# Kernel optimization log

Measured on AMD Instinct MI355X. Metric: run time of the kernel, lower is better.

## Reference

```python
import jax, jax.numpy as jnp
import numpy as np

LN_EPS = 1e-5        # torch default LayerNorm eps
DEB_EPS = 1e-7       # deberta-v3 layer_norm_eps
ATT_SPAN = 256       # deberta-v3-base position_buckets -> pos_ebd_size
MAX_REL = 100        # config.max_relative_positions override


def _ln(x, g, b, eps):
    m = x.mean(-1, keepdims=True)
    v = jnp.var(x, axis=-1, keepdims=True)
    return (x - m) * jax.lax.rsqrt(v + eps) * g + b


def _lin(x, w, b):
    return x @ w.T + b


def _rel_buckets(L):
    # build_relative_position + make_log_bucket_position (bucket_size=256, max_position=100)
    rel = jnp.arange(L, dtype=jnp.int32)[:, None] - jnp.arange(L, dtype=jnp.int32)[None, :]
    mid = ATT_SPAN // 2
    sign = jnp.sign(rel)
    abs_pos = jnp.where((rel < mid) & (rel > -mid), mid - 1, jnp.abs(rel))
    log_pos = jnp.ceil(jnp.log(abs_pos.astype(jnp.float32) / mid)
                       / np.float32(np.log((MAX_REL - 1) / mid)) * (mid - 1)) + mid
    return jnp.where(abs_pos <= mid, rel, (log_pos * sign).astype(jnp.int32))


def _forward(ints, floats):
    type_ids, landmark_ids, mask = ints
    (xs, ys, zs, type_emb, landmark_emb, type_ln_g, type_ln_b, lm_ln_g, lm_ln_b,
     pos_w, pos_b, lt_in_w, lt_in_b, lt_out_w, lt_out_b, lt_ln1_g, lt_ln1_b,
     lt_ff1_w, lt_ff1_b, lt_ff2_w, lt_ff2_b, lt_ln2_g, lt_ln2_b,
     rel_emb, rel_ln_g, rel_ln_b, dq_w, dq_b, dk_w, dk_b, dv_w, dv_b,
     dao_w, dao_b, da_ln_g, da_ln_b, di_w, di_b, do_w, do_b, do_ln_g, do_ln_b,
     head_w, head_b) = floats

    # embeddings (padding_idx=0 -> zero row & zero grad) + layernorms + pos projection
    te = _ln(type_emb[type_ids] * (type_ids != 0)[..., None].astype(jnp.float32), type_ln_g, type_ln_b, LN_EPS)
    le = _ln(landmark_emb[landmark_ids] * (landmark_ids != 0)[..., None].astype(jnp.float32), lm_ln_g, lm_ln_b, LN_EPS)
    pe = _lin(jnp.stack([xs, ys, zs], -1), pos_w, pos_b)
    fts = jnp.concatenate([te, le, pe], -1)                  # [B,F,L,768]
    B, F, L, D = fts.shape
    h = fts.reshape(B * F, L, D)

    # --- nn.TransformerEncoderLayer over landmarks (post-norm, relu, nhead=1) ---
    q, k, v = jnp.split(_lin(h, lt_in_w, lt_in_b), 3, axis=-1)
    probs = jax.nn.softmax(jnp.einsum('bqd,bkd->bqk', q, k) / np.float32(np.sqrt(D)), axis=-1)
    attn = _lin(jnp.einsum('bqk,bkd->bqd', probs, v), lt_out_w, lt_out_b)
    h = _ln(h + attn, lt_ln1_g, lt_ln1_b, LN_EPS)
    ff = _lin(jax.nn.relu(_lin(h, lt_ff1_w, lt_ff1_b)), lt_ff2_w, lt_ff2_b)
    h = _ln(h + ff, lt_ln2_g, lt_ln2_b, LN_EPS)

    h = h.reshape(B, F, L, D).mean(2)                        # [B,F,768]

    # --- DebertaV2 layer over frames (disentangled attention, 1 head) ---
    m = mask[:, :, 0] > 0                                    # [B,F]
    q = _lin(h, dq_w, dq_b)
    k = _lin(h, dk_w, dk_b)
    v = _lin(h, dv_w, dv_b)
    scale = np.float32(np.sqrt(D * 3))                       # scale_factor = 1 + len({c2p,p2c})
    scores = jnp.einsum('bqd,bkd->bqk', q, k) / scale
    rel_ln = _ln(rel_emb, rel_ln_g, rel_ln_b, DEB_EPS)       # norm_rel_ebd='layer_norm'
    pos_q = _lin(rel_ln, dq_w, dq_b)                         # share_att_key=True
    pos_k = _lin(rel_ln, dk_w, dk_b)
    rel = _rel_buckets(F)                                    # [F,F]
    c2p_idx = jnp.clip(rel + ATT_SPAN, 0, 2 * ATT_SPAN - 1)
    c2p = jnp.einsum('bqd,rd->bqr', q, pos_k)                # [B,F,512]
    c2p = jnp.take_along_axis(c2p, jnp.broadcast_to(c2p_idx[None], (B, F, F)), axis=-1)
    p2c_idx = jnp.clip(-rel + ATT_SPAN, 0, 2 * ATT_SPAN - 1)
    p2c = jnp.einsum('bkd,rd->bkr', k, pos_q)                # [B,F,512]
    p2c = jnp.take_along_axis(p2c, jnp.broadcast_to(p2c_idx[None], (B, F, F)), axis=-1)
    scores = scores + (c2p + jnp.swapaxes(p2c, -1, -2)) / scale
    amask = m[:, :, None] & m[:, None, :]                    # XSoftmax mask
    probs = jax.nn.softmax(jnp.where(amask, scores, jnp.finfo(scores.dtype).min), axis=-1)
    probs = jnp.where(amask, probs, 0.0)
    ctx = jnp.einsum('bqk,bkd->bqd', probs, v)
    h = _ln(_lin(ctx, dao_w, dao_b) + h, da_ln_g, da_ln_b, DEB_EPS)
    inter = jax.nn.gelu(_lin(h, di_w, di_b), approximate=False)
    h = _ln(_lin(inter, do_w, do_b) + h, do_ln_g, do_ln_b, DEB_EPS)

    return _lin(h.mean(1), head_w, head_b)                   # [B,250]


def setup_inputs():
    ks = iter(jax.random.split(jax.random.key(0), 64))
    B, F, L, E, D, DF, NC = 8, 80, 100, 256, 768, 3072, 250
    def w(*shape):
        return jax.random.normal(next(ks), shape, dtype=jnp.float32) * 0.02
    z = lambda *s: jnp.zeros(s, jnp.float32)
    o = lambda *s: jnp.ones(s, jnp.float32)
    return {
        "type_ids": jax.random.randint(next(ks), (B, F, L), 0, 12, dtype=jnp.int32),
        "landmark_ids": jax.random.randint(next(ks), (B, F, L), 0, 127, dtype=jnp.int32),
        "xs": jax.random.normal(next(ks), (B, F, L), dtype=jnp.float32),
        "ys": jax.random.normal(next(ks), (B, F, L), dtype=jnp.float32),
        "zs": jax.random.normal(next(ks), (B, F, L), dtype=jnp.float32),
        "mask": jnp.ones((B, F, L), jnp.int32),
        "type_emb": w(12, E), "landmark_emb": w(127, E),
        "type_ln_g": o(E), "type_ln_b": z(E), "lm_ln_g": o(E), "lm_ln_b": z(E),
        "pos_w": w(E, 3), "pos_b": z(E),
        "lt_in_w": w(3 * D, D), "lt_in_b": z(3 * D), "lt_out_w": w(D, D), "lt_out_b": z(D),
        "lt_ln1_g": o(D), "lt_ln1_b": z(D),
        "lt_ff1_w": w(D, D), "lt_ff1_b": z(D), "lt_ff2_w": w(D, D), "lt_ff2_b": z(D),
        "lt_ln2_g": o(D), "lt_ln2_b": z(D),
        "rel_emb": w(2 * ATT_SPAN, D), "rel_ln_g": o(D), "rel_ln_b": z(D),
        "dq_w": w(D, D), "dq_b": z(D), "dk_w": w(D, D), "dk_b": z(D), "dv_w": w(D, D), "dv_b": z(D),
        "dao_w": w(D, D), "dao_b": z(D), "da_ln_g": o(D), "da_ln_b": z(D),
        "di_w": w(DF, D), "di_b": z(DF), "do_w": w(D, DF), "do_b": z(D),
        "do_ln_g": o(D), "do_ln_b": z(D),
        "head_w": w(NC, D), "head_b": z(NC),
    }


def reference(type_ids, landmark_ids, xs, ys, zs, mask, type_emb, landmark_emb,
              type_ln_g, type_ln_b, lm_ln_g, lm_ln_b, pos_w, pos_b,
              lt_in_w, lt_in_b, lt_out_w, lt_out_b, lt_ln1_g, lt_ln1_b,
              lt_ff1_w, lt_ff1_b, lt_ff2_w, lt_ff2_b, lt_ln2_g, lt_ln2_b,
              rel_emb, rel_ln_g, rel_ln_b, dq_w, dq_b, dk_w, dk_b, dv_w, dv_b,
              dao_w, dao_b, da_ln_g, da_ln_b, di_w, di_b, do_w, do_b,
              do_ln_g, do_ln_b, head_w, head_b):
    floats = (xs, ys, zs, type_emb, landmark_emb, type_ln_g, type_ln_b, lm_ln_g, lm_ln_b,
              pos_w, pos_b, lt_in_w, lt_in_b, lt_out_w, lt_out_b, lt_ln1_g, lt_ln1_b,
              lt_ff1_w, lt_ff1_b, lt_ff2_w, lt_ff2_b, lt_ln2_g, lt_ln2_b,
              rel_emb, rel_ln_g, rel_ln_b, dq_w, dq_b, dk_w, dk_b, dv_w, dv_b,
              dao_w, dao_b, da_ln_g, da_ln_b, di_w, di_b, do_w, do_b, do_ln_g, do_ln_b,
              head_w, head_b)
    return _forward((type_ids, landmark_ids, mask), floats)
```

## Files before the change

kernel.cpp:

```cpp
#include <hip/hip_runtime.h>

using short8v = __attribute__((ext_vector_type(8))) short;
using float4v = __attribute__((ext_vector_type(4))) float;

__device__ __forceinline__ unsigned short f2bf(float f) {
  unsigned int u = __float_as_uint(f);
  u += 0x7FFF + ((u >> 16) & 1);
  return (unsigned short)(u >> 16);
}
__device__ __forceinline__ float bf2f(unsigned short u) {
  return __uint_as_float((unsigned int)u << 16);
}

__device__ __forceinline__ int swz(int row, int c) {
  return row * 64 + (c ^ ((row & 7) << 3));
}

template<int BM, int ACT, bool OUTBF, int RES>
__global__ __launch_bounds__(256) void gemm_mfma(
    const unsigned short* __restrict__ A, const unsigned short* __restrict__ B,
    const float* __restrict__ bias, const void* __restrict__ resid, int ldr,
    void* __restrict__ Cv,
    int M, int N, int K, int lda, int ldb, int ldc,
    long long sA, long long sB, long long sC, long long sBias, float alpha)
{
  constexpr int NF = BM / 32;
  A += (long long)blockIdx.z * sA;
  B += (long long)blockIdx.z * sB;
  if (bias) bias += (long long)blockIdx.z * sBias;
  const int m0 = blockIdx.y * BM, n0 = blockIdx.x * BM;

  __shared__ __align__(16) unsigned short As[BM * 64];
  __shared__ __align__(16) unsigned short Bs[BM * 64];

  const int tid = threadIdx.x;
  const int w = tid >> 6, lane = tid & 63;
  const int wr = w >> 1, wc = w & 1;

  const int r0 = tid >> 3;
  const int c8 = (tid & 7) * 8;
  int ra[NF], rb[NF], soff[NF];
  #pragma unroll
  for (int i = 0; i < NF; ++i) {
    int r = m0 + r0 + i * 32; ra[i] = r < M - 1 ? r : M - 1;
    int q = n0 + r0 + i * 32; rb[i] = q < N - 1 ? q : N - 1;
    soff[i] = swz(r0 + i * 32, c8);
  }

  const int fr = lane & 15;
  const int fk = (lane >> 4) * 8;

  float4v acc[NF][NF] = {};

  short8v pa[NF], pb[NF];
  #pragma unroll
  for (int i = 0; i < NF; ++i) {
    pa[i] = *(const short8v*)(A + (long long)ra[i] * lda + c8);
    pb[i] = *(const short8v*)(B + (long long)rb[i] * ldb + c8);
  }

  for (int k0 = 0; k0 < K; k0 += 64) {
    __syncthreads();
    #pragma unroll
    for (int i = 0; i < NF; ++i) {
      *(short8v*)&As[soff[i]] = pa[i];
      *(short8v*)&Bs[soff[i]] = pb[i];
    }
    __syncthreads();
    if (k0 + 64 < K) {
      #pragma unroll
      for (int i = 0; i < NF; ++i) {
        pa[i] = *(const short8v*)(A + (long long)ra[i] * lda + k0 + 64 + c8);
        pb[i] = *(const short8v*)(B + (long long)rb[i] * ldb + k0 + 64 + c8);
      }
    }
    #pragma unroll
    for (int kk = 0; kk < 2; ++kk) {
      short8v a[NF], b[NF];
      #pragma unroll
      for (int i = 0; i < NF; ++i) {
        a[i] = *(const short8v*)&As[swz(wr * (NF * 16) + i * 16 + fr, kk * 32 + fk)];
        b[i] = *(const short8v*)&Bs[swz(wc * (NF * 16) + i * 16 + fr, kk * 32 + fk)];
      }
      #pragma unroll
      for (int mi = 0; mi < NF; ++mi)
        #pragma unroll
        for (int ni = 0; ni < NF; ++ni)
          acc[mi][ni] = __builtin_amdgcn_mfma_f32_16x16x32_bf16(a[mi], b[ni], acc[mi][ni], 0, 0, 0);
    }
  }

  const int ccol0 = n0 + wc * (NF * 16) + (lane & 15);
  const int crow0 = m0 + wr * (NF * 16) + (lane >> 4) * 4;
  float* Cf = (float*)Cv + (long long)blockIdx.z * sC;
  unsigned short* Cb = (unsigned short*)Cv + (long long)blockIdx.z * sC;
  #pragma unroll
  for (int ni = 0; ni < NF; ++ni) {
    const int col = ccol0 + ni * 16;
    if (col >= N) continue;
    const float bs = bias ? bias[col] : 0.f;
    #pragma unroll
    for (int mi = 0; mi < NF; ++mi) {
      #pragma unroll
      for (int r = 0; r < 4; ++r) {
        const int row = crow0 + mi * 16 + r;
        if (row >= M) continue;
        float v = acc[mi][ni][r] * alpha + bs;
        if (RES == 1) v += bf2f(((const unsigned short*)resid)[(long long)row * ldr + col]);
        if (RES == 2) v += ((const float*)resid)[(long long)row * ldr + col];
        if (ACT == 1) v = fmaxf(v, 0.f);
        if (ACT == 2) v = 0.5f * v * (1.f + erff(v * 0.70710678118654752f));
        if (OUTBF) Cb[(long long)row * ldc + col] = f2bf(v);
        else       Cf[(long long)row * ldc + col] = v;
      }
    }
  }
}

static void mg(hipStream_t st, int bm, int act, bool outbf, int res,
               const unsigned short* A, const unsigned short* B,
               const float* bias, const void* resid, int ldr, void* C,
               int M, int N, int K, int lda, int ldb, int ldc,
               long long sA, long long sB, long long sC, long long sBias,
               int bat, float alpha)
{
  dim3 grid((N + bm - 1) / bm, (M + bm - 1) / bm, bat);
  dim3 blk(256);
  #define GEMM_CALL(BM_, A_, O_, R_) \
    gemm_mfma<BM_, A_, O_, R_><<<grid, blk, 0, st>>>(A, B, bias, resid, ldr, C, \
        M, N, K, lda, ldb, ldc, sA, sB, sC, sBias, alpha)
  if (bm == 128) {
    if (outbf) {
      if (act == 1)       GEMM_CALL(128, 1, true, 0);
      else if (res == 1)  GEMM_CALL(128, 0, true, 1);
      else                GEMM_CALL(128, 0, true, 0);
    } else {
      GEMM_CALL(128, 0, false, 0);
    }
  } else {
    if (outbf) {
      if (act == 2)       GEMM_CALL(64, 2, true, 0);
      else                GEMM_CALL(64, 0, true, 0);
    } else {
      if (res == 2)       GEMM_CALL(64, 0, false, 2);
      else                GEMM_CALL(64, 0, false, 0);
    }
  }
  #undef GEMM_CALL
}

__global__ __launch_bounds__(256) void scoresm_kernel(
    const unsigned short* __restrict__ Q, const unsigned short* __restrict__ Kp,
    unsigned short* __restrict__ P,
    int Mv, int K, int lda, long long sQ, long long sP, float alpha)
{
  const int z = blockIdx.z;
  Q  += (long long)z * sQ;
  Kp += (long long)z * sQ;
  P  += (long long)z * sP;

  __shared__ __align__(16) unsigned short As[128 * 64];
  __shared__ __align__(16) unsigned short Bs[128 * 64];
  float* ovl = (float*)As;

  const int tid = threadIdx.x;
  const int w = tid >> 6, lane = tid & 63;
  const int wr = w >> 1, wc = w & 1;
  const int r0 = tid >> 3, c8 = (tid & 7) * 8;

  int ra[4], soff[4];
  #pragma unroll
  for (int i = 0; i < 4; ++i) {
    int r = r0 + i * 32;
    ra[i] = (r < Mv - 1 ? r : Mv - 1);
    soff[i] = swz(r, c8);
  }
  const int fr = lane & 15, fk = (lane >> 4) * 8;

  float4v acc[4][4] = {};
  short8v pa[4], pb[4];
  #pragma unroll
  for (int i = 0; i < 4; ++i) {
    pa[i] = *(const short8v*)(Q  + (long long)ra[i] * lda + c8);
    pb[i] = *(const short8v*)(Kp + (long long)ra[i] * lda + c8);
  }
  for (int k0 = 0; k0 < K; k0 += 64) {
    __syncthreads();
    #pragma unroll
    for (int i = 0; i < 4; ++i) {
      *(short8v*)&As[soff[i]] = pa[i];
      *(short8v*)&Bs[soff[i]] = pb[i];
    }
    __syncthreads();
    if (k0 + 64 < K) {
      #pragma unroll
      for (int i = 0; i < 4; ++i) {
        pa[i] = *(const short8v*)(Q  + (long long)ra[i] * lda + k0 + 64 + c8);
        pb[i] = *(const short8v*)(Kp + (long long)ra[i] * lda + k0 + 64 + c8);
      }
    }
    #pragma unroll
    for (int kk = 0; kk < 2; ++kk) {
      short8v a[4], b[4];
      #pragma unroll
      for (int i = 0; i < 4; ++i) {
        a[i] = *(const short8v*)&As[swz(wr * 64 + i * 16 + fr, kk * 32 + fk)];
        b[i] = *(const short8v*)&Bs[swz(wc * 64 + i * 16 + fr, kk * 32 + fk)];
      }
      #pragma unroll
      for (int mi = 0; mi < 4; ++mi)
        #pragma unroll
        for (int ni = 0; ni < 4; ++ni)
          acc[mi][ni] = __builtin_amdgcn_mfma_f32_16x16x32_bf16(a[mi], b[ni], acc[mi][ni], 0, 0, 0);
    }
  }
  __syncthreads();

  const int g = lane >> 4, f = lane & 15;
  const int colB = wc * 64 + f;
  const int rowB = wr * 64 + g * 4;

  bool cv[4];
  #pragma unroll
  for (int ni = 0; ni < 4; ++ni) cv[ni] = (colB + ni * 16) < Mv;

  float lm[4][4];
  #pragma unroll
  for (int mi = 0; mi < 4; ++mi) {
    #pragma unroll
    for (int r = 0; r < 4; ++r) {
      float mx = -3.4e38f;
      #pragma unroll
      for (int ni = 0; ni < 4; ++ni) {
        float v = cv[ni] ? acc[mi][ni][r] * alpha : -3.4e38f;
        acc[mi][ni][r] = v;
        mx = fmaxf(mx, v);
      }
      #pragma unroll
      for (int off = 1; off < 16; off <<= 1) mx = fmaxf(mx, __shfl_xor(mx, off, 64));
      lm[mi][r] = mx;
    }
  }
  if (f == 0) {
    #pragma unroll
    for (int mi = 0; mi < 4; ++mi)
      #pragma unroll
      for (int r = 0; r < 4; ++r)
        ovl[wc * 128 + rowB + mi * 16 + r] = lm[mi][r];
  }
  __syncthreads();
  float ls[4][4];
  #pragma unroll
  for (int mi = 0; mi < 4; ++mi) {
    #pragma unroll
    for (int r = 0; r < 4; ++r) {
      const int row = rowB + mi * 16 + r;
      const float m = fmaxf(lm[mi][r], ovl[(wc ^ 1) * 128 + row]);
      float s = 0.f;
      #pragma unroll
      for (int ni = 0; ni < 4; ++ni) {
        const float v = acc[mi][ni][r];
        const float e = (v > -1e37f) ? expf(v - m) : 0.f;
        acc[mi][ni][r] = e;
        s += e;
      }
      #pragma unroll
      for (int off = 1; off < 16; off <<= 1) s += __shfl_xor(s, off, 64);
      ls[mi][r] = s;
    }
  }
  if (f == 0) {
    #pragma unroll
    for (int mi = 0; mi < 4; ++mi)
      #pragma unroll
      for (int r = 0; r < 4; ++r)
        ovl[256 + wc * 128 + rowB + mi * 16 + r] = ls[mi][r];
  }
  __syncthreads();
  #pragma unroll
  for (int mi = 0; mi < 4; ++mi) {
    #pragma unroll
    for (int r = 0; r < 4; ++r) {
      const int row = rowB + mi * 16 + r;
      const float tot = ls[mi][r] + ovl[256 + (wc ^ 1) * 128 + row];
      const float inv = (tot > 0.f) ? 1.f / tot : 0.f;
      #pragma unroll
      for (int ni = 0; ni < 4; ++ni)
        P[(long long)row * 128 + colB + ni * 16] = f2bf(acc[mi][ni][r] * inv);
    }
  }
}

struct ConvArgs {
  const float* s[10];
  unsigned short* d[10];
  long long off[11];
};
__global__ __launch_bounds__(256) void convall_kernel(ConvArgs a, long long tot)
{
  const long long i = ((long long)blockIdx.x * 256 + threadIdx.x) * 4;
  if (i >= tot) return;
  int t = 0;
  while (i >= a.off[t + 1]) ++t;
  const long long j = i - a.off[t];
  const float4 v = *(const float4*)(a.s[t] + j);
  const unsigned int lo = (unsigned int)f2bf(v.x) | ((unsigned int)f2bf(v.y) << 16);
  const unsigned int hi = (unsigned int)f2bf(v.z) | ((unsigned int)f2bf(v.w) << 16);
  *(uint2*)(a.d[t] + j) = make_uint2(lo, hi);
}

__global__ __launch_bounds__(256) void embed_kernel(
    const int* __restrict__ tids, const int* __restrict__ lids,
    const float* __restrict__ xs, const float* __restrict__ ys, const float* __restrict__ zs,
    const float* __restrict__ temb, const float* __restrict__ lemb,
    const float* __restrict__ tg, const float* __restrict__ tb,
    const float* __restrict__ lg, const float* __restrict__ lb,
    const float* __restrict__ pw, const float* __restrict__ pb,
    unsigned short* __restrict__ hb)
{
  const int tok = blockIdx.x * 4 + (threadIdx.x >> 6);
  const int lane = threadIdx.x & 63;
  const int e0 = lane * 4;
  const int ti = tids[tok], li = lids[tok];
  float4 tv = make_float4(0.f, 0.f, 0.f, 0.f);
  float4 lv = make_float4(0.f, 0.f, 0.f, 0.f);
  if (ti != 0) tv = *(const float4*)(temb + ti * 256 + e0);
  if (li != 0) lv = *(const float4*)(lemb + li * 256 + e0);

  float s0 = tv.x + tv.y + tv.z + tv.w;
  float s1 = tv.x * tv.x + tv.y * tv.y + tv.z * tv.z + tv.w * tv.w;
  float s2 = lv.x + lv.y + lv.z + lv.w;
  float s3 = lv.x * lv.x + lv.y * lv.y + lv.z * lv.z + lv.w * lv.w;
  #pragma unroll
  for (int off = 32; off > 0; off >>= 1) {
    s0 += __shfl_xor(s0, off, 64);
    s1 += __shfl_xor(s1, off, 64);
    s2 += __shfl_xor(s2, off, 64);
    s3 += __shfl_xor(s3, off, 64);
  }
  const float mt = s0 * (1.f / 256.f), vt = s1 * (1.f / 256.f) - mt * mt;
  const float ml = s2 * (1.f / 256.f), vl = s3 * (1.f / 256.f) - ml * ml;
  const float rt = rsqrtf(vt + 1e-5f), rl = rsqrtf(vl + 1e-5f);

  const float4 tg4 = *(const float4*)(tg + e0), tb4 = *(const float4*)(tb + e0);
  const float4 lg4 = *(const float4*)(lg + e0), lb4 = *(const float4*)(lb + e0);
  const size_t base = (size_t)tok * 768;
  ushort4 o;
  o.x = f2bf((tv.x - mt) * rt * tg4.x + tb4.x);
  o.y = f2bf((tv.y - mt) * rt * tg4.y + tb4.y);
  o.z = f2bf((tv.z - mt) * rt * tg4.z + tb4.z);
  o.w = f2bf((tv.w - mt) * rt * tg4.w + tb4.w);
  *(ushort4*)(hb + base + e0) = o;
  o.x = f2bf((lv.x - ml) * rl * lg4.x + lb4.x);
  o.y = f2bf((lv.y - ml) * rl * lg4.y + lb4.y);
  o.z = f2bf((lv.z - ml) * rl * lg4.z + lb4.z);
  o.w = f2bf((lv.w - ml) * rl * lg4.w + lb4.w);
  *(ushort4*)(hb + base + 256 + e0) = o;

  const float X = xs[tok], Y = ys[tok], Z = zs[tok];
  const float4 w0 = *(const float4*)(pw + 12 * lane);
  const float4 w1 = *(const float4*)(pw + 12 * lane + 4);
  const float4 w2 = *(const float4*)(pw + 12 * lane + 8);
  const float4 pb4 = *(const float4*)(pb + e0);
  o.x = f2bf(w0.x * X + w0.y * Y + w0.z * Z + pb4.x);
  o.y = f2bf(w0.w * X + w1.x * Y + w1.y * Z + pb4.y);
  o.z = f2bf(w1.z * X + w1.w * Y + w2.x * Z + pb4.z);
  o.w = f2bf(w2.y * X + w2.z * Y + w2.w * Z + pb4.w);
  *(ushort4*)(hb + base + 512 + e0) = o;
}

template<int XBF, int RBF>
__global__ __launch_bounds__(256) void ln_kernel(
    const void* __restrict__ x, const void* __restrict__ res,
    const float* __restrict__ g, const float* __restrict__ b,
    float* __restrict__ yf, unsigned short* __restrict__ yb,
    int nrows, float eps)
{
  const int row = blockIdx.x * 4 + (threadIdx.x >> 6);
  if (row >= nrows) return;
  const int lane = threadIdx.x & 63;
  const size_t base = (size_t)row * 768;
  const int e0 = lane * 12;
  float v[12];
  #pragma unroll
  for (int j = 0; j < 3; ++j) {
    if (XBF) {
      const ushort4 u = *(const ushort4*)((const unsigned short*)x + base + e0 + 4 * j);
      v[4*j+0] = bf2f(u.x); v[4*j+1] = bf2f(u.y); v[4*j+2] = bf2f(u.z); v[4*j+3] = bf2f(u.w);
    } else {
      const float4 fx = *(const float4*)((const float*)x + base + e0 + 4 * j);
      v[4*j+0] = fx.x; v[4*j+1] = fx.y; v[4*j+2] = fx.z; v[4*j+3] = fx.w;
    }
  }
  if (res) {
    #pragma unroll
    for (int j = 0; j < 3; ++j) {
      if (RBF) {
        const ushort4 u = *(const ushort4*)((const unsigned short*)res + base + e0 + 4 * j);
        v[4*j+0] += bf2f(u.x); v[4*j+1] += bf2f(u.y); v[4*j+2] += bf2f(u.z); v[4*j+3] += bf2f(u.w);
      } else {
        const float4 fx = *(const float4*)((const float*)res + base + e0 + 4 * j);
        v[4*j+0] += fx.x; v[4*j+1] += fx.y; v[4*j+2] += fx.z; v[4*j+3] += fx.w;
      }
    }
  }
  float s = 0.f, ss = 0.f;
  #pragma unroll
  for (int j = 0; j < 12; ++j) { s += v[j]; ss += v[j] * v[j]; }
  #pragma unroll
  for (int off = 32; off > 0; off >>= 1) {
    s += __shfl_xor(s, off, 64);
    ss += __shfl_xor(ss, off, 64);
  }
  const float mean = s * (1.f / 768.f);
  const float rstd = rsqrtf(ss * (1.f / 768.f) - mean * mean + eps);
  #pragma unroll
  for (int j = 0; j < 3; ++j) {
    const float4 g4 = *(const float4*)(g + e0 + 4 * j);
    const float4 b4 = *(const float4*)(b + e0 + 4 * j);
    float o0 = (v[4*j+0] - mean) * rstd * g4.x + b4.x;
    float o1 = (v[4*j+1] - mean) * rstd * g4.y + b4.y;
    float o2 = (v[4*j+2] - mean) * rstd * g4.z + b4.z;
    float o3 = (v[4*j+3] - mean) * rstd * g4.w + b4.w;
    if (yf) *(float4*)(yf + base + e0 + 4 * j) = make_float4(o0, o1, o2, o3);
    if (yb) {
      ushort4 u; u.x = f2bf(o0); u.y = f2bf(o1); u.z = f2bf(o2); u.w = f2bf(o3);
      *(ushort4*)(yb + base + e0 + 4 * j) = u;
    }
  }
}

__global__ __launch_bounds__(256) void vtrans_kernel(
    const unsigned short* __restrict__ v, unsigned short* __restrict__ vt,
    int Lk, int rs, long long sIn, long long sOut)
{
  __shared__ unsigned short s[64][132];
  const int b = blockIdx.y, d0 = blockIdx.x * 64;
  const unsigned short* vb = v + (long long)b * sIn;
  unsigned short* ob = vt + (long long)b * sOut;
  for (int idx = threadIdx.x; idx < 128 * 64; idx += 256) {
    const int k = idx >> 6, dd = idx & 63;
    s[dd][k] = (k < Lk) ? vb[(long long)k * rs + d0 + dd] : (unsigned short)0;
  }
  __syncthreads();
  for (int idx = threadIdx.x; idx < 64 * 128; idx += 256) {
    const int dd = idx >> 7, k = idx & 127;
    ob[(long long)(d0 + dd) * 128 + k] = s[dd][k];
  }
}

__global__ __launch_bounds__(256) void deb3_kernel(
    const float* __restrict__ sc,
    const float* __restrict__ c2p,
    const float* __restrict__ p2c,
    const int* __restrict__ mask,
    unsigned short* __restrict__ probs)
{
  const int rid = blockIdx.x * 4 + (threadIdx.x >> 6);
  if (rid >= 640) return;
  const int b = rid / 80, q = rid - b * 80;
  const int lane = threadIdx.x & 63;
  const bool mq = mask[(size_t)rid * 100] > 0;
  float v0 = -3.4e38f, v1 = -3.4e38f;
  bool val0 = false, val1 = false;
  {
    const int k = lane;
    const bool mk = mask[(size_t)(b * 80 + k) * 100] > 0;
    val0 = mq && mk;
    const int r = 256 + q - k;
    if (val0)
      v0 = sc[(size_t)b * 16384 + (size_t)q * 128 + k] +
           (c2p[(size_t)rid * 512 + r] + p2c[(size_t)(b * 80 + k) * 512 + r]) * (1.f / 48.f);
  }
  if (lane + 64 < 80) {
    const int k = lane + 64;
    const bool mk = mask[(size_t)(b * 80 + k) * 100] > 0;
    val1 = mq && mk;
    const int r = 256 + q - k;
    if (val1)
      v1 = sc[(size_t)b * 16384 + (size_t)q * 128 + k] +
           (c2p[(size_t)rid * 512 + r] + p2c[(size_t)(b * 80 + k) * 512 + r]) * (1.f / 48.f);
  }
  float m = fmaxf(v0, v1);
  #pragma unroll
  for (int off = 32; off > 0; off >>= 1) m = fmaxf(m, __shfl_xor(m, off, 64));
  const float e0 = val0 ? expf(v0 - m) : 0.f;
  const float e1 = val1 ? expf(v1 - m) : 0.f;
  float s = e0 + e1;
  #pragma unroll
  for (int off = 32; off > 0; off >>= 1) s += __shfl_xor(s, off, 64);
  const float inv = (s > 0.f) ? 1.f / s : 0.f;
  unsigned short* orow = probs + (size_t)b * 16384 + (size_t)q * 128;
  orow[lane] = val0 ? f2bf(e0 * inv) : (unsigned short)0;
  orow[lane + 64] = val1 ? f2bf(e1 * inv) : (unsigned short)0;
}

__global__ __launch_bounds__(192) void meanL_kernel(
    const unsigned short* __restrict__ hb, float* __restrict__ hf,
    unsigned short* __restrict__ hfb)
{
  const int bf = blockIdx.x;
  const int d0 = threadIdx.x * 4;
  float4 acc = make_float4(0.f, 0.f, 0.f, 0.f);
  for (int l = 0; l < 100; ++l) {
    const ushort4 u = *(const ushort4*)(hb + ((size_t)bf * 100 + l) * 768 + d0);
    acc.x += bf2f(u.x); acc.y += bf2f(u.y); acc.z += bf2f(u.z); acc.w += bf2f(u.w);
  }
  acc.x *= 0.01f; acc.y *= 0.01f; acc.z *= 0.01f; acc.w *= 0.01f;
  *(float4*)(hf + (size_t)bf * 768 + d0) = acc;
  ushort4 o; o.x = f2bf(acc.x); o.y = f2bf(acc.y); o.z = f2bf(acc.z); o.w = f2bf(acc.w);
  *(ushort4*)(hfb + (size_t)bf * 768 + d0) = o;
}

__global__ __launch_bounds__(192) void meanF_kernel(const float* __restrict__ h4, float* __restrict__ hm)
{
  const int b = blockIdx.x;
  const int d0 = threadIdx.x * 4;
  float4 acc = make_float4(0.f, 0.f, 0.f, 0.f);
  for (int f = 0; f < 80; ++f) {
    const float4 u = *(const float4*)(h4 + ((size_t)b * 80 + f) * 768 + d0);
    acc.x += u.x; acc.y += u.y; acc.z += u.z; acc.w += u.w;
  }
  const float k = 1.f / 80.f;
  *(float4*)(hm + (size_t)b * 768 + d0) = make_float4(acc.x * k, acc.y * k, acc.z * k, acc.w * k);
}

__global__ __launch_bounds__(64) void head_kernel(
    const float* __restrict__ hm, const float* __restrict__ w,
    const float* __restrict__ bias, float* __restrict__ out)
{
  const int n = blockIdx.x, b = blockIdx.y;
  const float* x = hm + (size_t)b * 768;
  const float* wn = w + (size_t)n * 768;
  float s = 0.f;
  for (int i = threadIdx.x * 4; i < 768; i += 256) {
    const float4 xv = *(const float4*)(x + i);
    const float4 wv = *(const float4*)(wn + i);
    s += xv.x * wv.x + xv.y * wv.y + xv.z * wv.z + xv.w * wv.w;
  }
  #pragma unroll
  for (int off = 32; off > 0; off >>= 1) s += __shfl_down(s, off, 64);
  if (threadIdx.x == 0) out[(size_t)b * 250 + n] = s + bias[n];
}

extern "C" void kernel_launch(void* const* d_in, const int* in_sizes, int n_in,
                              void* d_out, int out_size, void* d_ws, size_t ws_size,
                              hipStream_t stream)
{
  const int*   type_ids   = (const int*)  d_in[0];
  const int*   lm_ids     = (const int*)  d_in[1];
  const float* xs         = (const float*)d_in[2];
  const float* ys         = (const float*)d_in[3];
  const float* zs         = (const float*)d_in[4];
  const int*   mask       = (const int*)  d_in[5];
  const float* type_emb   = (const float*)d_in[6];
  const float* lm_emb     = (const float*)d_in[7];
  const float* type_ln_g  = (const float*)d_in[8];
  const float* type_ln_b  = (const float*)d_in[9];
  const float* lm_ln_g    = (const float*)d_in[10];
  const float* lm_ln_b    = (const float*)d_in[11];
  const float* pos_w      = (const float*)d_in[12];
  const float* pos_b      = (const float*)d_in[13];
  const float* lt_in_w    = (const float*)d_in[14];
  const float* lt_in_b    = (const float*)d_in[15];
  const float* lt_out_w   = (const float*)d_in[16];
  const float* lt_out_b   = (const float*)d_in[17];
  const float* lt_ln1_g   = (const float*)d_in[18];
  const float* lt_ln1_b   = (const float*)d_in[19];
  const float* lt_ff1_w   = (const float*)d_in[20];
  const float* lt_ff1_b   = (const float*)d_in[21];
  const float* lt_ff2_w   = (const float*)d_in[22];
  const float* lt_ff2_b   = (const float*)d_in[23];
  const float* lt_ln2_g   = (const float*)d_in[24];
  const float* lt_ln2_b   = (const float*)d_in[25];
  const float* rel_emb    = (const float*)d_in[26];
  const float* rel_ln_g   = (const float*)d_in[27];
  const float* rel_ln_b   = (const float*)d_in[28];
  const float* dq_w       = (const float*)d_in[29];
  const float* dq_b       = (const float*)d_in[30];
  const float* dk_w       = (const float*)d_in[31];
  const float* dk_b       = (const float*)d_in[32];
  const float* dv_w       = (const float*)d_in[33];
  const float* dv_b       = (const float*)d_in[34];
  const float* dao_w      = (const float*)d_in[35];
  const float* dao_b      = (const float*)d_in[36];
  const float* da_ln_g    = (const float*)d_in[37];
  const float* da_ln_b    = (const float*)d_in[38];
  const float* di_w       = (const float*)d_in[39];
  const float* di_b       = (const float*)d_in[40];
  const float* do_w       = (const float*)d_in[41];
  const float* do_b       = (const float*)d_in[42];
  const float* do_ln_g    = (const float*)d_in[43];
  const float* do_ln_b    = (const float*)d_in[44];
  const float* head_w     = (const float*)d_in[45];
  const float* head_b     = (const float*)d_in[46];
  float* out = (float*)d_out;
  float* ws  = (float*)d_ws;

  const float inv_sqrt_d = 0.03608439182435161f;
  const long long W2 = 768 * 768;

  auto rnd = [](size_t x) { return (x + 63) & ~(size_t)63; };
  const size_t ws_floats = ws_size / sizeof(float);

  size_t o = 0;
  const size_t offHB = o; o += rnd((size_t)64000 * 768 / 2);
  auto woff = [&](size_t elems) { size_t r = o; o += rnd(elems / 2); return r; };
  const size_t w_in   = woff((size_t)2304 * 768);
  const size_t w_out  = woff((size_t)768 * 768);
  const size_t w_f1   = woff((size_t)768 * 768);
  const size_t w_f2   = woff((size_t)768 * 768);
  const size_t w_qkv3 = woff((size_t)2304 * 768);
  const size_t w_ao   = woff((size_t)768 * 768);
  const size_t w_di   = woff((size_t)3072 * 768);
  const size_t w_do   = woff((size_t)768 * 3072);
  const size_t b_qkv3 = o; o += rnd(2304);
  const size_t scratch0 = o;

  size_t s3need = 0;
  {
    size_t t = 0;
    t += rnd((size_t)640 * 768);
    t += rnd((size_t)1152 * 768 / 2);
    t += rnd((size_t)1152 * 2304 / 2);
    t += 2 * (size_t)640 * 512;
    t += rnd((size_t)8 * 16384);
    t += rnd((size_t)8 * 16384 / 2);
    t += rnd((size_t)8 * 98304 / 2);
    t += rnd((size_t)640 * 768 / 2);
    t += 2 * rnd((size_t)640 * 768);
    t += rnd((size_t)640 * 768 / 2);
    t += rnd((size_t)640 * 3072 / 2);
    t += 2 * rnd((size_t)640 * 768);
    t += rnd((size_t)8 * 768);
    s3need = t;
  }

  auto chunk_need = [&](int c) {
    const size_t R = (size_t)c * 100;
    size_t t = 0;
    t += rnd(R * 2304 / 2);
    t += 4 * rnd(R * 768 / 2);
    t += rnd((size_t)c * 98304 / 2);
    t += rnd((size_t)c * 16384 / 2);
    return t;
  };
  int C = 1;
  {
    const int cands[] = {640, 320, 160, 80, 40, 20, 10, 5, 2, 1};
    for (int c : cands) {
      const size_t need = scratch0 + (chunk_need(c) > s3need ? chunk_need(c) : s3need);
      if (need <= ws_floats) { C = c; break; }
    }
  }
  const size_t R = (size_t)C * 100;

  o = scratch0;
  const size_t qkvb = o; o += rnd(R * 2304 / 2);
  const size_t ctxb = o; o += rnd(R * 768 / 2);
  const size_t t1b  = o; o += rnd(R * 768 / 2);
  const size_t h1bb = o; o += rnd(R * 768 / 2);
  const size_t ffob = o; o += rnd(R * 768 / 2);
  const size_t vtb  = o; o += rnd((size_t)C * 98304 / 2);
  const size_t pbf  = o; o += rnd((size_t)C * 16384 / 2);

  auto US = [&](size_t foff) { return (unsigned short*)(ws + foff); };

  {
    ConvArgs a;
    const float* srcs[10] = {lt_in_w, lt_out_w, lt_ff1_w, lt_ff2_w,
                             dq_w, dk_w, dv_w, dao_w, di_w, do_w};
    unsigned short* dsts[10] = {US(w_in), US(w_out), US(w_f1), US(w_f2),
                                US(w_qkv3), US(w_qkv3) + W2, US(w_qkv3) + 2 * W2,
                                US(w_ao), US(w_di), US(w_do)};
    const long long ns[10] = {2304 * 768, W2, W2, W2, W2, W2, W2, W2,
                              3072 * 768, 3072 * 768};
    long long tot = 0;
    for (int i = 0; i < 10; ++i) { a.s[i] = srcs[i]; a.d[i] = dsts[i]; a.off[i] = tot; tot += ns[i]; }
    a.off[10] = tot;
    convall_kernel<<<(unsigned)((tot / 4 + 255) / 256), 256, 0, stream>>>(a, tot);
  }
  hipMemcpyAsync(ws + b_qkv3,        dq_b, 768 * sizeof(float), hipMemcpyDeviceToDevice, stream);
  hipMemcpyAsync(ws + b_qkv3 + 768,  dk_b, 768 * sizeof(float), hipMemcpyDeviceToDevice, stream);
  hipMemcpyAsync(ws + b_qkv3 + 1536, dv_b, 768 * sizeof(float), hipMemcpyDeviceToDevice, stream);

  embed_kernel<<<16000, 256, 0, stream>>>(type_ids, lm_ids, xs, ys, zs,
      type_emb, lm_emb, type_ln_g, type_ln_b, lm_ln_g, lm_ln_b, pos_w, pos_b,
      US(offHB));

  for (int c0 = 0; c0 < 640; c0 += C) {
    unsigned short* hbc = US(offHB) + (size_t)c0 * 100 * 768;
    const int Rr = C * 100;
    mg(stream, 128, 0, true, 0, hbc, US(w_in), lt_in_b, nullptr, 0, US(qkvb),
       Rr, 2304, 768, 768, 768, 2304, 0, 0, 0, 0, 1, 1.f);
    scoresm_kernel<<<dim3(1, 1, C), 256, 0, stream>>>(
        US(qkvb), US(qkvb) + 768, US(pbf), 100, 768, 2304, 230400, 16384, inv_sqrt_d);
    vtrans_kernel<<<dim3(12, C), 256, 0, stream>>>(US(qkvb) + 1536, US(vtb), 100, 2304, 230400, 98304);
    mg(stream, 128, 0, true, 0, US(pbf), US(vtb), nullptr, nullptr, 0, US(ctxb),
       100, 768, 128, 128, 128, 768, 16384, 98304, 76800, 0, C, 1.f);
    mg(stream, 128, 0, true, 1, US(ctxb), US(w_out), lt_out_b, hbc, 768, US(t1b),
       Rr, 768, 768, 768, 768, 768, 0, 0, 0, 0, 1, 1.f);
    ln_kernel<1, 1><<<(Rr + 3) / 4, 256, 0, stream>>>(US(t1b), nullptr,
        lt_ln1_g, lt_ln1_b, nullptr, US(h1bb), Rr, 1e-5f);
    mg(stream, 128, 1, true, 0, US(h1bb), US(w_f1), lt_ff1_b, nullptr, 0, US(ffob),
       Rr, 768, 768, 768, 768, 768, 0, 0, 0, 0, 1, 1.f);
    mg(stream, 128, 0, true, 1, US(ffob), US(w_f2), lt_ff2_b, US(h1bb), 768, US(t1b),
       Rr, 768, 768, 768, 768, 768, 0, 0, 0, 0, 1, 1.f);
    ln_kernel<1, 1><<<(Rr + 3) / 4, 256, 0, stream>>>(US(t1b), nullptr,
        lt_ln2_g, lt_ln2_b, nullptr, hbc, Rr, 1e-5f);
  }

  o = scratch0;
  const size_t hf    = o; o += rnd((size_t)640 * 768);
  const size_t hfbE  = o; o += rnd((size_t)1152 * 768 / 2);
  const size_t qp    = o; o += rnd((size_t)1152 * 2304 / 2);
  const size_t c2p   = o; o += (size_t)640 * 512;
  const size_t p2c   = o; o += (size_t)640 * 512;
  const size_t p32_3 = o; o += rnd((size_t)8 * 16384);
  const size_t p3bf  = o; o += rnd((size_t)8 * 16384 / 2);
  const size_t vt3b  = o; o += rnd((size_t)8 * 98304 / 2);
  const size_t ctx3b = o; o += rnd((size_t)640 * 768 / 2);
  const size_t t3    = o; o += rnd((size_t)640 * 768);
  const size_t h3    = o; o += rnd((size_t)640 * 768);
  const size_t h3b   = o; o += rnd((size_t)640 * 768 / 2);
  const size_t interb= o; o += rnd((size_t)640 * 3072 / 2);
  const size_t t4    = o; o += rnd((size_t)640 * 768);
  const size_t h4    = o; o += rnd((size_t)640 * 768);
  const size_t hm    = o; o += rnd((size_t)8 * 768);

  meanL_kernel<<<640, 192, 0, stream>>>(US(offHB), ws + hf, US(hfbE));
  ln_kernel<0, 0><<<128, 256, 0, stream>>>(rel_emb, nullptr,
      rel_ln_g, rel_ln_b, nullptr, US(hfbE) + (size_t)640 * 768, 512, 1e-7f);
  mg(stream, 64, 0, true, 0, US(hfbE), US(w_qkv3), ws + b_qkv3, nullptr, 0, US(qp),
     1152, 2304, 768, 768, 768, 2304, 0, 0, 0, 0, 1, 1.f);
  mg(stream, 64, 0, false, 0, US(qp), US(qp) + 768, nullptr, nullptr, 0, ws + p32_3,
     80, 80, 768, 2304, 2304, 128, 184320, 184320, 16384, 0, 8, 1.f / 48.f);
  mg(stream, 64, 0, false, 0, US(qp), US(qp) + (size_t)640 * 2304 + 768, nullptr, nullptr, 0, ws + c2p,
     640, 512, 768, 2304, 2304, 512, 768, -768, 327680, 0, 2, 1.f);
  deb3_kernel<<<160, 256, 0, stream>>>(ws + p32_3, ws + c2p, ws + p2c, mask, US(p3bf));
  vtrans_kernel<<<dim3(12, 8), 256, 0, stream>>>(US(qp) + 1536, US(vt3b), 80, 2304, 184320, 98304);
  mg(stream, 64, 0, true, 0, US(p3bf), US(vt3b), nullptr, nullptr, 0, US(ctx3b),
     80, 768, 128, 128, 128, 768, 16384, 98304, 61440, 0, 8, 1.f);
  mg(stream, 64, 0, false, 2, US(ctx3b), US(w_ao), dao_b, ws + hf, 768, ws + t3,
     640, 768, 768, 768, 768, 768, 0, 0, 0, 0, 1, 1.f);
  ln_kernel<0, 0><<<160, 256, 0, stream>>>(ws + t3, nullptr,
      da_ln_g, da_ln_b, ws + h3, US(h3b), 640, 1e-7f);
  mg(stream, 64, 2, true, 0, US(h3b), US(w_di), di_b, nullptr, 0, US(interb),
     640, 3072, 768, 768, 768, 3072, 0, 0, 0, 0, 1, 1.f);
  mg(stream, 64, 0, false, 2, US(interb), US(w_do), do_b, ws + h3, 768, ws + t4,
     640, 768, 3072, 3072, 3072, 768, 0, 0, 0, 0, 1, 1.f);
  ln_kernel<0, 0><<<160, 256, 0, stream>>>(ws + t4, nullptr,
      do_ln_g, do_ln_b, ws + h4, nullptr, 640, 1e-7f);
  meanF_kernel<<<8, 192, 0, stream>>>(ws + h4, ws + hm);
  head_kernel<<<dim3(250, 8), 64, 0, stream>>>(ws + hm, head_w, head_b, out);
}
```

Baseline: 1.950 ms.

## Fuse V transpose into QKV GEMM epilogue and add XCD-aware block remapping

The QKV projection GEMM now writes its V columns directly in transposed layout into the per-batch V^T buffer, which removes the separate vtrans kernels. The padding region is zeroed once per buffer with a memset instead of on every transpose. In addition, every GEMM with 64 or more workgroups remaps block IDs so that consecutive tiles land on the same XCD, aiming for better L2 reuse. The transposed stores are strided, uncoalesced 2-byte writes, which may cost bandwidth in the epilogue.

```diff
diff --git a/kernel.cpp b/kernel.cpp
--- a/kernel.cpp
+++ b/kernel.cpp
@@ -16,11 +16,11 @@
   return row * 64 + (c ^ ((row & 7) << 3));
 }
 
-template<int BM, int ACT, bool OUTBF, int RES>
+template<int BM, int ACT, bool OUTBF, int RES, int VT>
 __global__ __launch_bounds__(256) void gemm_mfma(
     const unsigned short* __restrict__ A, const unsigned short* __restrict__ B,
     const float* __restrict__ bias, const void* __restrict__ resid, int ldr,
-    void* __restrict__ Cv,
+    void* __restrict__ Cv, unsigned short* __restrict__ vtp, int vrows, int vmax,
     int M, int N, int K, int lda, int ldb, int ldc,
     long long sA, long long sB, long long sC, long long sBias, float alpha)
 {
@@ -28,7 +28,17 @@
   A += (long long)blockIdx.z * sA;
   B += (long long)blockIdx.z * sB;
   if (bias) bias += (long long)blockIdx.z * sBias;
-  const int m0 = blockIdx.y * BM, n0 = blockIdx.x * BM;
+
+  int bx = blockIdx.x, by = blockIdx.y;
+  const int nwg = gridDim.x * gridDim.y;
+  if (nwg >= 64) {
+    const int bid = by * gridDim.x + bx;
+    const int q = nwg >> 3, r = nwg & 7;
+    const int xcd = bid & 7, idx = bid >> 3;
+    const int nbid = (xcd < r ? xcd * (q + 1) : r * (q + 1) + (xcd - r) * q) + idx;
+    by = nbid / gridDim.x; bx = nbid - by * gridDim.x;
+  }
+  const int m0 = by * BM, n0 = bx * BM;
 
   __shared__ __align__(16) unsigned short As[BM * 64];
   __shared__ __align__(16) unsigned short Bs[BM * 64];
@@ -110,8 +120,17 @@
         if (RES == 2) v += ((const float*)resid)[(long long)row * ldr + col];
         if (ACT == 1) v = fmaxf(v, 0.f);
         if (ACT == 2) v = 0.5f * v * (1.f + erff(v * 0.70710678118654752f));
-        if (OUTBF) Cb[(long long)row * ldc + col] = f2bf(v);
-        else       Cf[(long long)row * ldc + col] = v;
+        if (VT && col >= 1536) {
+          if (row < vmax) {
+            const int bq = row / vrows;
+            const int kk2 = row - bq * vrows;
+            vtp[(long long)bq * 98304 + (long long)(col - 1536) * 128 + kk2] = f2bf(v);
+          }
+        } else if (OUTBF) {
+          Cb[(long long)row * ldc + col] = f2bf(v);
+        } else {
+          Cf[(long long)row * ldc + col] = v;
+        }
       }
     }
   }
@@ -120,30 +139,33 @@
 static void mg(hipStream_t st, int bm, int act, bool outbf, int res,
                const unsigned short* A, const unsigned short* B,
                const float* bias, const void* resid, int ldr, void* C,
+               unsigned short* vtp, int vrows, int vmax,
                int M, int N, int K, int lda, int ldb, int ldc,
                long long sA, long long sB, long long sC, long long sBias,
                int bat, float alpha)
 {
   dim3 grid((N + bm - 1) / bm, (M + bm - 1) / bm, bat);
   dim3 blk(256);
-  #define GEMM_CALL(BM_, A_, O_, R_) \
-    gemm_mfma<BM_, A_, O_, R_><<<grid, blk, 0, st>>>(A, B, bias, resid, ldr, C, \
-        M, N, K, lda, ldb, ldc, sA, sB, sC, sBias, alpha)
+  #define GEMM_CALL(BM_, A_, O_, R_, V_) \
+    gemm_mfma<BM_, A_, O_, R_, V_><<<grid, blk, 0, st>>>(A, B, bias, resid, ldr, C, \
+        vtp, vrows, vmax, M, N, K, lda, ldb, ldc, sA, sB, sC, sBias, alpha)
   if (bm == 128) {
     if (outbf) {
-      if (act == 1)       GEMM_CALL(128, 1, true, 0);
-      else if (res == 1)  GEMM_CALL(128, 0, true, 1);
-      else                GEMM_CALL(128, 0, true, 0);
+      if (act == 1)       GEMM_CALL(128, 1, true, 0, 0);
+      else if (res == 1)  GEMM_CALL(128, 0, true, 1, 0);
+      else if (vtp)       GEMM_CALL(128, 0, true, 0, 1);
+      else                GEMM_CALL(128, 0, true, 0, 0);
     } else {
-      GEMM_CALL(128, 0, false, 0);
+      GEMM_CALL(128, 0, false, 0, 0);
     }
   } else {
     if (outbf) {
-      if (act == 2)       GEMM_CALL(64, 2, true, 0);
-      else                GEMM_CALL(64, 0, true, 0);
+      if (act == 2)       GEMM_CALL(64, 2, true, 0, 0);
+      else if (vtp)       GEMM_CALL(64, 0, true, 0, 1);
+      else                GEMM_CALL(64, 0, true, 0, 0);
     } else {
-      if (res == 2)       GEMM_CALL(64, 0, false, 2);
-      else                GEMM_CALL(64, 0, false, 0);
+      if (res == 2)       GEMM_CALL(64, 0, false, 2, 0);
+      else                GEMM_CALL(64, 0, false, 0, 0);
     }
   }
   #undef GEMM_CALL
@@ -427,25 +449,6 @@
       ushort4 u; u.x = f2bf(o0); u.y = f2bf(o1); u.z = f2bf(o2); u.w = f2bf(o3);
       *(ushort4*)(yb + base + e0 + 4 * j) = u;
     }
-  }
-}
-
-__global__ __launch_bounds__(256) void vtrans_kernel(
-    const unsigned short* __restrict__ v, unsigned short* __restrict__ vt,
-    int Lk, int rs, long long sIn, long long sOut)
-{
-  __shared__ unsigned short s[64][132];
-  const int b = blockIdx.y, d0 = blockIdx.x * 64;
-  const unsigned short* vb = v + (long long)b * sIn;
-  unsigned short* ob = vt + (long long)b * sOut;
-  for (int idx = threadIdx.x; idx < 128 * 64; idx += 256) {
-    const int k = idx >> 6, dd = idx & 63;
-    s[dd][k] = (k < Lk) ? vb[(long long)k * rs + d0 + dd] : (unsigned short)0;
-  }
-  __syncthreads();
-  for (int idx = threadIdx.x; idx < 64 * 128; idx += 256) {
-    const int dd = idx >> 7, k = idx & 127;
-    ob[(long long)(d0 + dd) * 128 + k] = s[dd][k];
   }
 }
 
@@ -688,23 +691,29 @@
       type_emb, lm_emb, type_ln_g, type_ln_b, lm_ln_g, lm_ln_b, pos_w, pos_b,
       US(offHB));
 
+  hipMemsetAsync(US(vtb), 0, (size_t)C * 98304 * sizeof(unsigned short), stream);
+
   for (int c0 = 0; c0 < 640; c0 += C) {
     unsigned short* hbc = US(offHB) + (size_t)c0 * 100 * 768;
     const int Rr = C * 100;
     mg(stream, 128, 0, true, 0, hbc, US(w_in), lt_in_b, nullptr, 0, US(qkvb),
+       US(vtb), 100, Rr,
        Rr, 2304, 768, 768, 768, 2304, 0, 0, 0, 0, 1, 1.f);
     scoresm_kernel<<<dim3(1, 1, C), 256, 0, stream>>>(
         US(qkvb), US(qkvb) + 768, US(pbf), 100, 768, 2304, 230400, 16384, inv_sqrt_d);
-    vtrans_kernel<<<dim3(12, C), 256, 0, stream>>>(US(qkvb) + 1536, US(vtb), 100, 2304, 230400, 98304);
     mg(stream, 128, 0, true, 0, US(pbf), US(vtb), nullptr, nullptr, 0, US(ctxb),
+       nullptr, 0, 0,
        100, 768, 128, 128, 128, 768, 16384, 98304, 76800, 0, C, 1.f);
     mg(stream, 128, 0, true, 1, US(ctxb), US(w_out), lt_out_b, hbc, 768, US(t1b),
+       nullptr, 0, 0,
        Rr, 768, 768, 768, 768, 768, 0, 0, 0, 0, 1, 1.f);
     ln_kernel<1, 1><<<(Rr + 3) / 4, 256, 0, stream>>>(US(t1b), nullptr,
         lt_ln1_g, lt_ln1_b, nullptr, US(h1bb), Rr, 1e-5f);
     mg(stream, 128, 1, true, 0, US(h1bb), US(w_f1), lt_ff1_b, nullptr, 0, US(ffob),
+       nullptr, 0, 0,
        Rr, 768, 768, 768, 768, 768, 0, 0, 0, 0, 1, 1.f);
     mg(stream, 128, 0, true, 1, US(ffob), US(w_f2), lt_ff2_b, US(h1bb), 768, US(t1b),
+       nullptr, 0, 0,
        Rr, 768, 768, 768, 768, 768, 0, 0, 0, 0, 1, 1.f);
     ln_kernel<1, 1><<<(Rr + 3) / 4, 256, 0, stream>>>(US(t1b), nullptr,
         lt_ln2_g, lt_ln2_b, nullptr, hbc, Rr, 1e-5f);
@@ -731,23 +740,30 @@
   meanL_kernel<<<640, 192, 0, stream>>>(US(offHB), ws + hf, US(hfbE));
   ln_kernel<0, 0><<<128, 256, 0, stream>>>(rel_emb, nullptr,
       rel_ln_g, rel_ln_b, nullptr, US(hfbE) + (size_t)640 * 768, 512, 1e-7f);
+  hipMemsetAsync(US(vt3b), 0, (size_t)8 * 98304 * sizeof(unsigned short), stream);
   mg(stream, 64, 0, true, 0, US(hfbE), US(w_qkv3), ws + b_qkv3, nullptr, 0, US(qp),
+     US(vt3b), 80, 640,
      1152, 2304, 768, 768, 768, 2304, 0, 0, 0, 0, 1, 1.f);
   mg(stream, 64, 0, false, 0, US(qp), US(qp) + 768, nullptr, nullptr, 0, ws + p32_3,
+     nullptr, 0, 0,
      80, 80, 768, 2304, 2304, 128, 184320, 184320, 16384, 0, 8, 1.f / 48.f);
   mg(stream, 64, 0, false, 0, US(qp), US(qp) + (size_t)640 * 2304 + 768, nullptr, nullptr, 0, ws + c2p,
+     nullptr, 0, 0,
      640, 512, 768, 2304, 2304, 512, 768, -768, 327680, 0, 2, 1.f);
   deb3_kernel<<<160, 256, 0, stream>>>(ws + p32_3, ws + c2p, ws + p2c, mask, US(p3bf));
-  vtrans_kernel<<<dim3(12, 8), 256, 0, stream>>>(US(qp) + 1536, US(vt3b), 80, 2304, 184320, 98304);
   mg(stream, 64, 0, true, 0, US(p3bf), US(vt3b), nullptr, nullptr, 0, US(ctx3b),
+     nullptr, 0, 0,
      80, 768, 128, 128, 128, 768, 16384, 98304, 61440, 0, 8, 1.f);
   mg(stream, 64, 0, false, 2, US(ctx3b), US(w_ao), dao_b, ws + hf, 768, ws + t3,
+     nullptr, 0, 0,
      640, 768, 768, 768, 768, 768, 0, 0, 0, 0, 1, 1.f);
   ln_kernel<0, 0><<<160, 256, 0, stream>>>(ws + t3, nullptr,
       da_ln_g, da_ln_b, ws + h3, US(h3b), 640, 1e-7f);
   mg(stream, 64, 2, true, 0, US(h3b), US(w_di), di_b, nullptr, 0, US(interb),
+     nullptr, 0, 0,
      640, 3072, 768, 768, 768, 3072, 0, 0, 0, 0, 1, 1.f);
   mg(stream, 64, 0, false, 2, US(interb), US(w_do), do_b, ws + h3, 768, ws + t4,
+     nullptr, 0, 0,
      640, 768, 3072, 3072, 3072, 768, 0, 0, 0, 0, 1, 1.f);
   ln_kernel<0, 0><<<160, 256, 0, stream>>>(ws + t4, nullptr,
       do_ln_g, do_ln_b, ws + h4, nullptr, 640, 1e-7f);
```

Measured after the change: 2.053 ms. 1.05x slower.
